# Kernel tuning notes

Measured on AMD Instinct MI355X. Metric: run time of the kernel, lower is better.

Reference implementation:

```python
import jax, jax.numpy as jnp
import numpy as np

T, V, D, L, H, F, R = 1024, 17, 1024, 2, 16, 4096, 32
DH = D // H
LORA_SCALE = 2.0  # lora_alpha / r = 64 / 32
MASK_ID = 16
NEG = jnp.float32(-1e9)


def setup_inputs() -> dict:
    key = jax.random.key(0)
    ks = iter(jax.random.split(key, 64))
    def p(shape, std):
        return jax.random.normal(next(ks), shape, jnp.float32) * std
    inp = {
        "packed_context": jax.random.randint(next(ks), (T,), 0, V),
        "cu_seq_lens": jnp.sort(jax.random.randint(next(ks), (5,), 0, T)),
        "max_seq_len": T,
        "row_coords": jax.random.randint(next(ks), (T,), 0, 64),
        "col_coords": jax.random.randint(next(ks), (T,), 0, 64),
        "num_diffusion_steps": 2,
        "E": p((V, D), 0.02),  # embed rows actually used: weight[:vocab_size]
    }
    shapes = {"q": (D, D), "k": (D, D), "v": (D, D), "o": (D, D),
              "g": (D, F), "u": (D, F), "d": (F, D)}
    for nm, (di, do) in shapes.items():
        inp["W" + nm] = p((L, di, do), di ** -0.5)  # frozen NF4 base weight (dequantized)
        inp["A" + nm] = p((L, di, R), di ** -0.5)   # LoRA A
        inp["B" + nm] = p((L, R, do), 0.01)          # LoRA B (nonzero for grad testing)
    inp["ln1"] = jnp.ones((L, D), jnp.float32)
    inp["ln2"] = jnp.ones((L, D), jnp.float32)
    inp["lnf"] = jnp.ones((D,), jnp.float32)
    return inp


def _rms(x, w):
    return x * jax.lax.rsqrt(jnp.mean(x * x, axis=-1, keepdims=True) + 1e-6) * w


def _lora(x, W, A, B):
    # fused base matmul + low-rank LoRA delta
    return x @ W + LORA_SCALE * ((x @ A) @ B)


def _denoise_step(soft, E, Wq, Aq, Bq, Wk, Ak, Bk, Wv, Av, Bv, Wo, Ao, Bo,
                  Wg, Ag, Bg, Wu, Au, Bu, Wd, Ad, Bd, ln1, ln2, lnf, causal_bias):
    # soft-token embedding: [T,V] @ [V,D]
    x = soft @ E
    inv_sqrt_dh = jnp.float32(1.0 / np.sqrt(DH))
    for l in range(L):
        h = _rms(x, ln1[l])
        q = _lora(h, Wq[l], Aq[l], Bq[l]).reshape(T, H, DH)
        k = _lora(h, Wk[l], Ak[l], Bk[l]).reshape(T, H, DH)
        v = _lora(h, Wv[l], Av[l], Bv[l]).reshape(T, H, DH)
        scores = jnp.einsum('qhd,khd->hqk', q, k) * inv_sqrt_dh + causal_bias
        att = jax.nn.softmax(scores, axis=-1)
        ctx = jnp.einsum('hqk,khd->qhd', att, v).reshape(T, D)
        x = x + _lora(ctx, Wo[l], Ao[l], Bo[l])
        h2 = _rms(x, ln2[l])
        ff = jax.nn.silu(_lora(h2, Wg[l], Ag[l], Bg[l])) * _lora(h2, Wu[l], Au[l], Bu[l])
        x = x + _lora(ff, Wd[l], Ad[l], Bd[l])
    logits = _rms(x, lnf) @ E.T  # tied head over the 17-token task vocab
    return jax.nn.softmax(logits, axis=-1)


def reference(packed_context, cu_seq_lens, max_seq_len, row_coords, col_coords,
              num_diffusion_steps, E, Wq, Aq, Bq, Wk, Ak, Bk, Wv, Av, Bv,
              Wo, Ao, Bo, Wg, Ag, Bg, Wu, Au, Bu, Wd, Ad, Bd, ln1, ln2, lnf):
    causal_bias = jnp.where(jnp.tril(jnp.ones((T, T), bool)), jnp.float32(0.0), NEG)
    is_prompt = (packed_context != MASK_ID)[:, None]  # [T,1]
    ctx_onehot = jax.nn.one_hot(packed_context, V, dtype=jnp.float32)
    soft = jnp.zeros((T, V), jnp.float32).at[:, MASK_ID].set(1.0)
    for _ in range(int(num_diffusion_steps)):
        refined = _denoise_step(soft, E, Wq, Aq, Bq, Wk, Ak, Bk, Wv, Av, Bv,
                                Wo, Ao, Bo, Wg, Ag, Bg, Wu, Au, Bu, Wd, Ad, Bd,
                                ln1, ln2, lnf, causal_bias)
        soft = jnp.where(is_prompt, ctx_onehot, refined)
    return jnp.argmax(soft, axis=-1)
```

## Files before the change

kernel.cpp:

```cpp
#include <hip/hip_runtime.h>
#include <hip/hip_bf16.h>

#define T_LEN 1024
#define D_DIM 1024
#define V_DIM 17
#define H_NUM 16
#define DH_DIM 64
#define F_DIM 4096
#define R_LORA 32
#define N_LAYERS 2
#define N_STEPS 2
#define MASK_ID 16
#define LORA_SCALE 2.0f

typedef __attribute__((ext_vector_type(8))) short bfx8;
typedef __attribute__((ext_vector_type(4))) float f32x4;

typedef unsigned short ushort_t;
typedef unsigned int uint_t;

#define AS1 __attribute__((address_space(1)))
#define AS3 __attribute__((address_space(3)))

__device__ __forceinline__ void gload16(const ushort_t* g, ushort_t* l) {
    __builtin_amdgcn_global_load_lds((const AS1 void*)(const void*)g,
                                     (AS3 void*)(void*)l, 16, 0, 0);
}

__device__ __forceinline__ ushort_t f2bf(float v) {
    __hip_bfloat16 h = __float2bfloat16(v);
    return __builtin_bit_cast(unsigned short, h);
}
__device__ __forceinline__ float bf2f(ushort_t u) {
    return __uint_as_float(((uint_t)u) << 16);
}
__device__ __forceinline__ void split4_store(float y0, float y1, float y2, float y3,
                                             ushort_t* __restrict__ hi, ushort_t* __restrict__ lo,
                                             size_t idx) {
    ushort_t h0 = f2bf(y0), h1 = f2bf(y1), h2 = f2bf(y2), h3 = f2bf(y3);
    ushort_t l0 = f2bf(y0 - bf2f(h0));
    ushort_t l1 = f2bf(y1 - bf2f(h1));
    ushort_t l2 = f2bf(y2 - bf2f(h2));
    ushort_t l3 = f2bf(y3 - bf2f(h3));
    uint2 hv, lv;
    hv.x = (uint_t)h0 | ((uint_t)h1 << 16);
    hv.y = (uint_t)h2 | ((uint_t)h3 << 16);
    lv.x = (uint_t)l0 | ((uint_t)l1 << 16);
    lv.y = (uint_t)l2 | ((uint_t)l3 << 16);
    *(uint2*)(hi + idx) = hv;
    *(uint2*)(lo + idx) = lv;
}

__global__ void init_soft_kernel(float* __restrict__ soft) {
    int idx = blockIdx.x * blockDim.x + threadIdx.x;
    if (idx < T_LEN * V_DIM) {
        soft[idx] = ((idx % V_DIM) == MASK_ID) ? 1.0f : 0.0f;
    }
}

__global__ __launch_bounds__(256) void embed_kernel(const float* __restrict__ soft,
                                                    const float* __restrict__ E,
                                                    float* __restrict__ x) {
    int t = blockIdx.x;
    __shared__ float srow[V_DIM];
    if (threadIdx.x < V_DIM) srow[threadIdx.x] = soft[t * V_DIM + threadIdx.x];
    __syncthreads();
    for (int d = threadIdx.x; d < D_DIM; d += 256) {
        float acc = 0.f;
        #pragma unroll
        for (int v = 0; v < V_DIM; v++) acc += srow[v] * E[v * D_DIM + d];
        x[(size_t)t * D_DIM + d] = acc;
    }
}

__global__ __launch_bounds__(256) void fold_kernel(
    const float* __restrict__ W,
    const float* __restrict__ A,
    const float* __restrict__ Bm,
    ushort_t* __restrict__ oHi,
    ushort_t* __restrict__ oLo,
    int K, int N)
{
    const int l = blockIdx.z;
    W   += (size_t)l * K * N;
    A   += (size_t)l * K * R_LORA;
    Bm  += (size_t)l * R_LORA * N;
    oHi += (size_t)l * K * N;
    oLo += (size_t)l * K * N;
    __shared__ uint_t tile[64][65];
    const int tid = threadIdx.x;
    const int n0 = blockIdx.x * 64, k0 = blockIdx.y * 64;
    {
        const int nl = tid & 63, kq = tid >> 6;
        float breg[R_LORA];
        #pragma unroll
        for (int r = 0; r < R_LORA; r++) breg[r] = Bm[(size_t)r * N + n0 + nl];
        for (int i = 0; i < 16; i++) {
            const int kl = kq * 16 + i;
            const size_t kgl = (size_t)(k0 + kl);
            const float* arow = A + kgl * R_LORA;
            float acc = 0.f;
            #pragma unroll
            for (int r = 0; r < R_LORA; r++) acc = fmaf(arow[r], breg[r], acc);
            float val = W[kgl * N + n0 + nl] + LORA_SCALE * acc;
            ushort_t h = f2bf(val);
            ushort_t l2 = f2bf(val - bf2f(h));
            tile[kl][nl] = ((uint_t)h << 16) | (uint_t)l2;
        }
    }
    __syncthreads();
    {
        const int kl = tid & 63, nb = tid >> 6;
        for (int i = 0; i < 16; i++) {
            const int nl = nb * 16 + i;
            uint_t pk = tile[kl][nl];
            size_t idx = (size_t)(n0 + nl) * K + k0 + kl;
            oHi[idx] = (ushort_t)(pk >> 16);
            oLo[idx] = (ushort_t)(pk & 0xffffu);
        }
    }
}

__global__ __launch_bounds__(256) void rms_split_kernel(
    const float* __restrict__ x, const float* __restrict__ w,
    ushort_t* __restrict__ hi, ushort_t* __restrict__ lo)
{
    const int t = blockIdx.x, tid = threadIdx.x;
    const float* xr = x + (size_t)t * D_DIM;
    float4 xv = *(const float4*)(xr + tid * 4);
    float ss = xv.x * xv.x + xv.y * xv.y + xv.z * xv.z + xv.w * xv.w;
    __shared__ float red[4];
    const int lane = tid & 63, wv = tid >> 6;
    #pragma unroll
    for (int off = 32; off > 0; off >>= 1) ss += __shfl_xor(ss, off);
    if (lane == 0) red[wv] = ss;
    __syncthreads();
    ss = red[0] + red[1] + red[2] + red[3];
    const float r = 1.0f / sqrtf(ss * (1.0f / D_DIM) + 1e-6f);
    const float4 wv4 = *(const float4*)(w + tid * 4);
    size_t base = (size_t)t * D_DIM + tid * 4;
    split4_store(xv.x * r * wv4.x, xv.y * r * wv4.y, xv.z * r * wv4.z, xv.w * r * wv4.w,
                 hi, lo, base);
}

struct GemmJob {
    const ushort_t* Bh;
    const ushort_t* Bl;
    float* Cf;
    ushort_t* Ch;
    ushort_t* Cl;
    int k0, k1;
};

__global__ __launch_bounds__(256) void gemm128_kernel(
    const ushort_t* __restrict__ Ahi, const ushort_t* __restrict__ Alo,
    int K, int N, GemmJob j0, GemmJob j1, GemmJob j2, GemmJob j3)
{
    GemmJob jb = (blockIdx.z == 0) ? j0 : (blockIdx.z == 1) ? j1 : (blockIdx.z == 2) ? j2 : j3;
    __shared__ ushort_t Ash[128][32];
    __shared__ ushort_t Asl[128][32];
    __shared__ ushort_t Bsh[128][32];
    __shared__ ushort_t Bsl[128][32];

    const int tid = threadIdx.x, lane = tid & 63, w = tid >> 6;
    const int l15 = lane & 15, lg = lane >> 4;
    const int m0 = blockIdx.y * 128, n0 = blockIdx.x * 128;
    const int wm = (w >> 1) * 64, wn = (w & 1) * 64;

    const int r0 = w * 32;
    const int rsub = lane >> 2;
    const int cs = lane & 3;
    const int csl = (cs ^ (rsub & 3)) * 8;
    const int rsl = (lg ^ (l15 & 3)) * 8;

    f32x4 acc[4][4];
    #pragma unroll
    for (int i = 0; i < 4; i++)
        #pragma unroll
        for (int j = 0; j < 4; j++) acc[i][j] = f32x4{0.f, 0.f, 0.f, 0.f};

    const size_t rowA = (size_t)(m0 + r0 + rsub) * K;
    const size_t rowB = (size_t)(n0 + r0 + rsub) * K;
    const size_t rstep = (size_t)16 * K;

    for (int kk = jb.k0; kk < jb.k1; kk += 32) {
        {
            const ushort_t* a0 = Ahi + rowA + kk + csl;
            const ushort_t* a1 = Alo + rowA + kk + csl;
            const ushort_t* b0 = jb.Bh + rowB + kk + csl;
            const ushort_t* b1 = jb.Bl + rowB + kk + csl;
            gload16(a0,         &Ash[r0][0]);
            gload16(a0 + rstep, &Ash[r0 + 16][0]);
            gload16(a1,         &Asl[r0][0]);
            gload16(a1 + rstep, &Asl[r0 + 16][0]);
            gload16(b0,         &Bsh[r0][0]);
            gload16(b0 + rstep, &Bsh[r0 + 16][0]);
            gload16(b1,         &Bsl[r0][0]);
            gload16(b1 + rstep, &Bsl[r0 + 16][0]);
        }
        __syncthreads();
        bfx8 bh[4], bl[4];
        #pragma unroll
        for (int ni = 0; ni < 4; ni++) {
            bh[ni] = *(const bfx8*)&Bsh[wn + ni * 16 + l15][rsl];
            bl[ni] = *(const bfx8*)&Bsl[wn + ni * 16 + l15][rsl];
        }
        #pragma unroll
        for (int mi = 0; mi < 4; mi++) {
            bfx8 ah = *(const bfx8*)&Ash[wm + mi * 16 + l15][rsl];
            bfx8 al = *(const bfx8*)&Asl[wm + mi * 16 + l15][rsl];
            #pragma unroll
            for (int ni = 0; ni < 4; ni++) {
                acc[mi][ni] = __builtin_amdgcn_mfma_f32_16x16x32_bf16(ah, bh[ni], acc[mi][ni], 0, 0, 0);
                acc[mi][ni] = __builtin_amdgcn_mfma_f32_16x16x32_bf16(ah, bl[ni], acc[mi][ni], 0, 0, 0);
                acc[mi][ni] = __builtin_amdgcn_mfma_f32_16x16x32_bf16(al, bh[ni], acc[mi][ni], 0, 0, 0);
            }
        }
        __syncthreads();
    }

    if (jb.Cf) {
        #pragma unroll
        for (int mi = 0; mi < 4; mi++)
            #pragma unroll
            for (int ni = 0; ni < 4; ni++) {
                int col = n0 + wn + ni * 16 + l15;
                #pragma unroll
                for (int i = 0; i < 4; i++) {
                    int row = m0 + wm + mi * 16 + lg * 4 + i;
                    jb.Cf[(size_t)row * N + col] = acc[mi][ni][i];
                }
            }
    } else {
        #pragma unroll
        for (int mi = 0; mi < 4; mi++)
            #pragma unroll
            for (int ni = 0; ni < 4; ni++) {
                int col = n0 + wn + ni * 16 + l15;
                #pragma unroll
                for (int i = 0; i < 4; i++) {
                    int row = m0 + wm + mi * 16 + lg * 4 + i;
                    size_t idx = (size_t)row * N + col;
                    float v = acc[mi][ni][i];
                    ushort_t h = f2bf(v);
                    jb.Ch[idx] = h;
                    jb.Cl[idx] = f2bf(v - bf2f(h));
                }
            }
    }
}

__global__ void add2_kernel(float* __restrict__ x, const float* __restrict__ p0,
                            const float* __restrict__ p1, int n4) {
    int i = blockIdx.x * blockDim.x + threadIdx.x;
    if (i < n4) {
        float4 xv = *(const float4*)(x + (size_t)i * 4);
        float4 a = *(const float4*)(p0 + (size_t)i * 4);
        float4 b = *(const float4*)(p1 + (size_t)i * 4);
        xv.x += a.x + b.x; xv.y += a.y + b.y; xv.z += a.z + b.z; xv.w += a.w + b.w;
        *(float4*)(x + (size_t)i * 4) = xv;
    }
}
__global__ void add4_kernel(float* __restrict__ x, const float* __restrict__ p0,
                            const float* __restrict__ p1, const float* __restrict__ p2,
                            const float* __restrict__ p3, int n4) {
    int i = blockIdx.x * blockDim.x + threadIdx.x;
    if (i < n4) {
        float4 xv = *(const float4*)(x + (size_t)i * 4);
        float4 a = *(const float4*)(p0 + (size_t)i * 4);
        float4 b = *(const float4*)(p1 + (size_t)i * 4);
        float4 c = *(const float4*)(p2 + (size_t)i * 4);
        float4 d = *(const float4*)(p3 + (size_t)i * 4);
        xv.x += a.x + b.x + c.x + d.x;
        xv.y += a.y + b.y + c.y + d.y;
        xv.z += a.z + b.z + c.z + d.z;
        xv.w += a.w + b.w + c.w + d.w;
        *(float4*)(x + (size_t)i * 4) = xv;
    }
}

#define KS_PAD 72
#define P_PAD 72
__global__ __launch_bounds__(256, 1) void attn_mfma_kernel(
    const ushort_t* __restrict__ qh, const ushort_t* __restrict__ ql,
    const ushort_t* __restrict__ kh, const ushort_t* __restrict__ kl,
    const ushort_t* __restrict__ vh, const ushort_t* __restrict__ vl,
    ushort_t* __restrict__ chi, ushort_t* __restrict__ clo)
{
    __shared__ ushort_t Ksh[64][KS_PAD];
    __shared__ ushort_t Ksl[64][KS_PAD];
    __shared__ ushort_t VTh[64][KS_PAD];
    __shared__ ushort_t VTl[64][KS_PAD];
    __shared__ ushort_t Ph[4][16][P_PAD];
    __shared__ ushort_t Pl[4][16][P_PAD];

    const int qt = blockIdx.x, hh = blockIdx.y;
    const int tid = threadIdx.x, w = tid >> 6, lane = tid & 63;
    const int l15 = lane & 15, lg = lane >> 4;
    const int q0 = qt * 64;
    const int hcol = hh * DH_DIM;

    bfx8 qa_h[2], qa_l[2];
    {
        size_t qrow = (size_t)(q0 + w * 16 + l15) * D_DIM + hcol;
        #pragma unroll
        for (int ks = 0; ks < 2; ks++) {
            qa_h[ks] = *(const bfx8*)(qh + qrow + ks * 32 + lg * 8);
            qa_l[ks] = *(const bfx8*)(ql + qrow + ks * 32 + lg * 8);
        }
    }

    f32x4 o[4];
    #pragma unroll
    for (int ni = 0; ni < 4; ni++) o[ni] = f32x4{0.f, 0.f, 0.f, 0.f};
    float mrun[4], lrun[4];
    #pragma unroll
    for (int i = 0; i < 4; i++) { mrun[i] = -3.0e38f; lrun[i] = 0.f; }

    const int srow = tid >> 2;
    const int sseg = (tid & 3) * 16;
    const int vp = tid & 31;
    const int vd0 = (tid >> 5) * 8;

    for (int kt = 0; kt <= qt; kt++) {
        __syncthreads();
        {
            size_t src = (size_t)(kt * 64 + srow) * D_DIM + hcol + sseg;
            *(uint4*)&Ksh[srow][sseg]     = *(const uint4*)(kh + src);
            *(uint4*)&Ksh[srow][sseg + 8] = *(const uint4*)(kh + src + 8);
            *(uint4*)&Ksl[srow][sseg]     = *(const uint4*)(kl + src);
            *(uint4*)&Ksl[srow][sseg + 8] = *(const uint4*)(kl + src + 8);
        }
        {
            size_t s0 = (size_t)(kt * 64 + 2 * vp) * D_DIM + hcol + vd0;
            uint4 h0 = *(const uint4*)(vh + s0);
            uint4 h1 = *(const uint4*)(vh + s0 + D_DIM);
            uint4 l0 = *(const uint4*)(vl + s0);
            uint4 l1 = *(const uint4*)(vl + s0 + D_DIM);
            const ushort_t* a = (const ushort_t*)&h0;
            const ushort_t* b = (const ushort_t*)&h1;
            const ushort_t* c = (const ushort_t*)&l0;
            const ushort_t* d = (const ushort_t*)&l1;
            #pragma unroll
            for (int j = 0; j < 8; j++) {
                *(uint_t*)&VTh[vd0 + j][2 * vp] = (uint_t)a[j] | ((uint_t)b[j] << 16);
                *(uint_t*)&VTl[vd0 + j][2 * vp] = (uint_t)c[j] | ((uint_t)d[j] << 16);
            }
        }
        __syncthreads();

        f32x4 s[4];
        #pragma unroll
        for (int ni = 0; ni < 4; ni++) s[ni] = f32x4{0.f, 0.f, 0.f, 0.f};
        #pragma unroll
        for (int ks = 0; ks < 2; ks++) {
            #pragma unroll
            for (int ni = 0; ni < 4; ni++) {
                bfx8 bh = *(const bfx8*)&Ksh[ni * 16 + l15][ks * 32 + lg * 8];
                bfx8 bl = *(const bfx8*)&Ksl[ni * 16 + l15][ks * 32 + lg * 8];
                s[ni] = __builtin_amdgcn_mfma_f32_16x16x32_bf16(qa_h[ks], bh, s[ni], 0, 0, 0);
                s[ni] = __builtin_amdgcn_mfma_f32_16x16x32_bf16(qa_h[ks], bl, s[ni], 0, 0, 0);
                s[ni] = __builtin_amdgcn_mfma_f32_16x16x32_bf16(qa_l[ks], bh, s[ni], 0, 0, 0);
            }
        }

        const int kbase = kt * 64;
        float rmax[4];
        #pragma unroll
        for (int i = 0; i < 4; i++) rmax[i] = -3.0e38f;
        #pragma unroll
        for (int ni = 0; ni < 4; ni++) {
            int kc = kbase + ni * 16 + l15;
            #pragma unroll
            for (int i = 0; i < 4; i++) {
                int qrow = q0 + w * 16 + lg * 4 + i;
                float v = s[ni][i] * 0.125f;
                v = (kc <= qrow) ? v : -3.0e38f;
                s[ni][i] = v;
                rmax[i] = fmaxf(rmax[i], v);
            }
        }
        #pragma unroll
        for (int off = 1; off < 16; off <<= 1) {
            #pragma unroll
            for (int i = 0; i < 4; i++) rmax[i] = fmaxf(rmax[i], __shfl_xor(rmax[i], off));
        }
        float psum[4];
        #pragma unroll
        for (int i = 0; i < 4; i++) {
            float nm = fmaxf(mrun[i], rmax[i]);
            float sc = __expf(mrun[i] - nm);
            lrun[i] *= sc;
            #pragma unroll
            for (int ni = 0; ni < 4; ni++) o[ni][i] *= sc;
            mrun[i] = nm;
            psum[i] = 0.f;
        }
        #pragma unroll
        for (int ni = 0; ni < 4; ni++) {
            #pragma unroll
            for (int i = 0; i < 4; i++) {
                float e = __expf(s[ni][i] - mrun[i]);
                s[ni][i] = e;
                psum[i] += e;
            }
        }
        #pragma unroll
        for (int off = 1; off < 16; off <<= 1) {
            #pragma unroll
            for (int i = 0; i < 4; i++) psum[i] += __shfl_xor(psum[i], off);
        }
        #pragma unroll
        for (int i = 0; i < 4; i++) lrun[i] += psum[i];

        #pragma unroll
        for (int ni = 0; ni < 4; ni++) {
            #pragma unroll
            for (int i = 0; i < 4; i++) {
                float e = s[ni][i];
                ushort_t hp = f2bf(e);
                Ph[w][lg * 4 + i][ni * 16 + l15] = hp;
                Pl[w][lg * 4 + i][ni * 16 + l15] = f2bf(e - bf2f(hp));
            }
        }
        #pragma unroll
        for (int ks = 0; ks < 2; ks++) {
            bfx8 ah = *(const bfx8*)&Ph[w][l15][ks * 32 + lg * 8];
            bfx8 al = *(const bfx8*)&Pl[w][l15][ks * 32 + lg * 8];
            #pragma unroll
            for (int ni = 0; ni < 4; ni++) {
                bfx8 bh = *(const bfx8*)&VTh[ni * 16 + l15][ks * 32 + lg * 8];
                bfx8 bl = *(const bfx8*)&VTl[ni * 16 + l15][ks * 32 + lg * 8];
                o[ni] = __builtin_amdgcn_mfma_f32_16x16x32_bf16(ah, bh, o[ni], 0, 0, 0);
                o[ni] = __builtin_amdgcn_mfma_f32_16x16x32_bf16(ah, bl, o[ni], 0, 0, 0);
                o[ni] = __builtin_amdgcn_mfma_f32_16x16x32_bf16(al, bh, o[ni], 0, 0, 0);
            }
        }
    }

    #pragma unroll
    for (int i = 0; i < 4; i++) {
        float inv = 1.0f / lrun[i];
        #pragma unroll
        for (int ni = 0; ni < 4; ni++) o[ni][i] *= inv;
    }
    #pragma unroll
    for (int ni = 0; ni < 4; ni++) {
        int col = hcol + ni * 16 + l15;
        #pragma unroll
        for (int i = 0; i < 4; i++) {
            int row = q0 + w * 16 + lg * 4 + i;
            size_t idx = (size_t)row * D_DIM + col;
            float v = o[ni][i];
            ushort_t hp = f2bf(v);
            chi[idx] = hp;
            clo[idx] = f2bf(v - bf2f(hp));
        }
    }
}

__global__ void silu_split_kernel(const float* __restrict__ g, const float* __restrict__ u,
                                  ushort_t* __restrict__ hi, ushort_t* __restrict__ lo, int n4) {
    int i = blockIdx.x * blockDim.x + threadIdx.x;
    if (i < n4) {
        float4 gv = *(const float4*)(g + (size_t)i * 4);
        float4 uv = *(const float4*)(u + (size_t)i * 4);
        float y0 = gv.x / (1.f + expf(-gv.x)) * uv.x;
        float y1 = gv.y / (1.f + expf(-gv.y)) * uv.y;
        float y2 = gv.z / (1.f + expf(-gv.z)) * uv.z;
        float y3 = gv.w / (1.f + expf(-gv.w)) * uv.w;
        split4_store(y0, y1, y2, y3, hi, lo, (size_t)i * 4);
    }
}

__global__ __launch_bounds__(256) void head_kernel(const float* __restrict__ x,
                                                   const float* __restrict__ lnf,
                                                   const float* __restrict__ E,
                                                   const int* __restrict__ tok,
                                                   float* __restrict__ soft) {
    int t = blockIdx.x;
    int tid = threadIdx.x;
    __shared__ float y[D_DIM];
    __shared__ float red[4];
    __shared__ float logits[V_DIM];
    const float* xr = x + (size_t)t * D_DIM;
    float ss = 0.f;
    for (int d = tid; d < D_DIM; d += 256) { float v = xr[d]; ss += v * v; }
    int lane = tid & 63, wave = tid >> 6;
    for (int off = 32; off > 0; off >>= 1) ss += __shfl_xor(ss, off);
    if (lane == 0) red[wave] = ss;
    __syncthreads();
    ss = red[0] + red[1] + red[2] + red[3];
    float r = 1.0f / sqrtf(ss * (1.0f / D_DIM) + 1e-6f);
    for (int d = tid; d < D_DIM; d += 256) y[d] = xr[d] * r * lnf[d];
    __syncthreads();
    for (int vv = wave; vv < V_DIM; vv += 4) {
        float p = 0.f;
        for (int d = lane; d < D_DIM; d += 64) p += y[d] * E[vv * D_DIM + d];
        for (int off = 32; off > 0; off >>= 1) p += __shfl_xor(p, off);
        if (lane == 0) logits[vv] = p;
    }
    __syncthreads();
    if (tid == 0) {
        int tk = tok[t];
        if (tk != MASK_ID) {
            for (int vv = 0; vv < V_DIM; vv++) soft[t * V_DIM + vv] = (vv == tk) ? 1.f : 0.f;
        } else {
            float mx = -1e30f;
            for (int vv = 0; vv < V_DIM; vv++) mx = fmaxf(mx, logits[vv]);
            float sm = 0.f;
            float e[V_DIM];
            for (int vv = 0; vv < V_DIM; vv++) { e[vv] = expf(logits[vv] - mx); sm += e[vv]; }
            float invs = 1.0f / sm;
            for (int vv = 0; vv < V_DIM; vv++) soft[t * V_DIM + vv] = e[vv] * invs;
        }
    }
}

__global__ void argmax_kernel(const float* __restrict__ soft, int* __restrict__ out) {
    int t = blockIdx.x * blockDim.x + threadIdx.x;
    if (t < T_LEN) {
        const float* s = soft + t * V_DIM;
        int best = 0;
        float bv = s[0];
        #pragma unroll
        for (int vv = 1; vv < V_DIM; vv++) {
            float v = s[vv];
            if (v > bv) { bv = v; best = vv; }
        }
        out[t] = best;
    }
}

__global__ __launch_bounds__(256) void rms_kernel(const float* __restrict__ x,
                                                  const float* __restrict__ w,
                                                  float* __restrict__ out) {
    int t = blockIdx.x;
    const float* xr = x + (size_t)t * D_DIM;
    float ss = 0.f;
    for (int d = threadIdx.x; d < D_DIM; d += 256) { float v = xr[d]; ss += v * v; }
    __shared__ float red[4];
    int lane = threadIdx.x & 63, wave = threadIdx.x >> 6;
    for (int off = 32; off > 0; off >>= 1) ss += __shfl_xor(ss, off);
    if (lane == 0) red[wave] = ss;
    __syncthreads();
    ss = red[0] + red[1] + red[2] + red[3];
    float r = 1.0f / sqrtf(ss * (1.0f / D_DIM) + 1e-6f);
    for (int d = threadIdx.x; d < D_DIM; d += 256) out[(size_t)t * D_DIM + d] = xr[d] * r * w[d];
}

__global__ __launch_bounds__(256) void gemm_kernel(const float* __restrict__ A,
                                                   const float* __restrict__ B,
                                                   float* __restrict__ C,
                                                   int M, int N, int K,
                                                   float alpha, int accumulate) {
    const int BM = 64, BN = 64, BK = 16;
    __shared__ float As[BK][BM];
    __shared__ float Bsh[BK][BN];
    int tid = threadIdx.x;
    int tx = tid % 16, ty = tid / 16;
    int row0 = blockIdx.y * BM, col0 = blockIdx.x * BN;
    float acc[4][4] = {};
    for (int k0 = 0; k0 < K; k0 += BK) {
        #pragma unroll
        for (int i = 0; i < 4; i++) {
            int e = tid * 4 + i;
            int m = e / BK, kk = e % BK;
            int gr = row0 + m, gk = k0 + kk;
            As[kk][m] = (gr < M && gk < K) ? A[(size_t)gr * K + gk] : 0.f;
        }
        #pragma unroll
        for (int i = 0; i < 4; i++) {
            int e = tid * 4 + i;
            int kk = e / BN, n = e % BN;
            int gk = k0 + kk, gc = col0 + n;
            Bsh[kk][n] = (gk < K && gc < N) ? B[(size_t)gk * N + gc] : 0.f;
        }
        __syncthreads();
        #pragma unroll
        for (int kk = 0; kk < BK; kk++) {
            float a[4], b[4];
            #pragma unroll
            for (int i = 0; i < 4; i++) a[i] = As[kk][ty * 4 + i];
            #pragma unroll
            for (int j = 0; j < 4; j++) b[j] = Bsh[kk][tx * 4 + j];
            #pragma unroll
            for (int i = 0; i < 4; i++)
                #pragma unroll
                for (int j = 0; j < 4; j++)
                    acc[i][j] += a[i] * b[j];
        }
        __syncthreads();
    }
    #pragma unroll
    for (int i = 0; i < 4; i++) {
        int r = row0 + ty * 4 + i;
        if (r >= M) continue;
        #pragma unroll
        for (int j = 0; j < 4; j++) {
            int c = col0 + tx * 4 + j;
            if (c >= N) continue;
            size_t idx = (size_t)r * N + c;
            float val = alpha * acc[i][j];
            if (accumulate) val += C[idx];
            C[idx] = val;
        }
    }
}

__global__ __launch_bounds__(256) void attn_kernel(const float* __restrict__ q,
                                                   const float* __restrict__ k,
                                                   const float* __restrict__ v,
                                                   float* __restrict__ ctx) {
    int qi = blockIdx.x;
    int hh = blockIdx.y;
    __shared__ float sc[T_LEN];
    __shared__ float qrow[DH_DIM];
    __shared__ float red[8];
    __shared__ float part[4][DH_DIM];
    int tid = threadIdx.x;
    int lane = tid & 63, wave = tid >> 6;
    const float* qp = q + (size_t)qi * D_DIM + hh * DH_DIM;
    if (tid < DH_DIM) qrow[tid] = qp[tid];
    __syncthreads();
    const float scale = 0.125f;
    for (int j = wave; j <= qi; j += 4) {
        const float* kp = k + (size_t)j * D_DIM + hh * DH_DIM;
        float p = qrow[lane] * kp[lane];
        for (int off = 32; off > 0; off >>= 1) p += __shfl_xor(p, off);
        if (lane == 0) sc[j] = p * scale;
    }
    __syncthreads();
    int n = qi + 1;
    float m = -1e30f;
    for (int j = tid; j < n; j += 256) m = fmaxf(m, sc[j]);
    for (int off = 32; off > 0; off >>= 1) m = fmaxf(m, __shfl_xor(m, off));
    if (lane == 0) red[wave] = m;
    __syncthreads();
    m = fmaxf(fmaxf(red[0], red[1]), fmaxf(red[2], red[3]));
    float s = 0.f;
    for (int j = tid; j < n; j += 256) { float e = expf(sc[j] - m); sc[j] = e; s += e; }
    for (int off = 32; off > 0; off >>= 1) s += __shfl_xor(s, off);
    if (lane == 0) red[4 + wave] = s;
    __syncthreads();
    s = red[4] + red[5] + red[6] + red[7];
    float inv = 1.0f / s;
    float acc = 0.f;
    for (int j = wave; j < n; j += 4) {
        acc += sc[j] * v[(size_t)j * D_DIM + hh * DH_DIM + lane];
    }
    part[wave][lane] = acc;
    __syncthreads();
    if (tid < DH_DIM) {
        float r = (part[0][tid] + part[1][tid] + part[2][tid] + part[3][tid]) * inv;
        ctx[(size_t)qi * D_DIM + hh * DH_DIM + tid] = r;
    }
}

__global__ void silu_mul_kernel(const float* __restrict__ g, const float* __restrict__ u,
                                float* __restrict__ out, int nelem) {
    int i = blockIdx.x * blockDim.x + threadIdx.x;
    if (i < nelem) {
        float gv = g[i];
        float sg = 1.0f / (1.0f + expf(-gv));
        out[i] = gv * sg * u[i];
    }
}

static inline void launch_gemm(const float* A, const float* B, float* C,
                               int M, int N, int K, float alpha, int accumulate,
                               hipStream_t stream) {
    dim3 grid((N + 63) / 64, (M + 63) / 64);
    gemm_kernel<<<grid, 256, 0, stream>>>(A, B, C, M, N, K, alpha, accumulate);
}

extern "C" void kernel_launch(void* const* d_in, const int* in_sizes, int n_in,
                              void* d_out, int out_size, void* d_ws, size_t ws_size,
                              hipStream_t stream) {
    const int* packed = (const int*)d_in[0];
    const float* E  = (const float*)d_in[6];
    const float* Wsrc[7] = {(const float*)d_in[7],  (const float*)d_in[10], (const float*)d_in[13],
                            (const float*)d_in[16], (const float*)d_in[19], (const float*)d_in[22],
                            (const float*)d_in[25]};
    const float* Asrc[7] = {(const float*)d_in[8],  (const float*)d_in[11], (const float*)d_in[14],
                            (const float*)d_in[17], (const float*)d_in[20], (const float*)d_in[23],
                            (const float*)d_in[26]};
    const float* Bsrc[7] = {(const float*)d_in[9],  (const float*)d_in[12], (const float*)d_in[15],
                            (const float*)d_in[18], (const float*)d_in[21], (const float*)d_in[24],
                            (const float*)d_in[27]};
    const float* ln1 = (const float*)d_in[28];
    const float* ln2 = (const float*)d_in[29];
    const float* lnf = (const float*)d_in[30];

    const size_t DD = (size_t)D_DIM * D_DIM;
    const size_t DF = (size_t)D_DIM * F_DIM;
    const size_t wsizes[7] = {DD, DD, DD, DD, DF, DF, DF};
    const int Kdim[7] = {D_DIM, D_DIM, D_DIM, D_DIM, D_DIM, D_DIM, F_DIM};
    const int Ndim[7] = {D_DIM, D_DIM, D_DIM, D_DIM, F_DIM, F_DIM, D_DIM};

    size_t u16_elems = 0;
    for (int p = 0; p < 7; p++) u16_elems += 2ull * N_LAYERS * wsizes[p];
    u16_elems += 2ull * DD;
    u16_elems += 2ull * DD;
    u16_elems += 2ull * DF;
    u16_elems += 6ull * DD;
    size_t f32_elems = (size_t)T_LEN * V_DIM + DD  + 2 * DF ;
    size_t need = u16_elems * 2 + f32_elems * 4 + 256;

    if (ws_size >= need) {
        ushort_t* ub = (ushort_t*)d_ws;
        size_t uo = 0;
        ushort_t *Whi[7], *Wlo[7];
        for (int p = 0; p < 7; p++) {
            Whi[p] = ub + uo; uo += (size_t)N_LAYERS * wsizes[p];
            Wlo[p] = ub + uo; uo += (size_t)N_LAYERS * wsizes[p];
        }
        ushort_t* h_hi = ub + uo; uo += DD;
        ushort_t* h_lo = ub + uo; uo += DD;
        ushort_t* c_hi = ub + uo; uo += DD;
        ushort_t* c_lo = ub + uo; uo += DD;
        ushort_t* f_hi = ub + uo; uo += DF;
        ushort_t* f_lo = ub + uo; uo += DF;
        ushort_t* qbh = ub + uo; uo += DD;
        ushort_t* qbl = ub + uo; uo += DD;
        ushort_t* kbh = ub + uo; uo += DD;
        ushort_t* kbl = ub + uo; uo += DD;
        ushort_t* vbh = ub + uo; uo += DD;
        ushort_t* vbl = ub + uo; uo += DD;
        float* fb = (float*)(ub + uo);
        size_t fo = 0;
        float* soft = fb + fo; fo += (size_t)T_LEN * V_DIM;
        float* x    = fb + fo; fo += DD;
        float* gbuf = fb + fo; fo += DF;
        float* ubuf = fb + fo; fo += DF;
        float* p0 = gbuf;
        float* p1 = gbuf + DD;
        float* p2 = gbuf + 2 * DD;
        float* p3 = gbuf + 3 * DD;

        for (int p = 0; p < 7; p++) {
            dim3 grid(Ndim[p] / 64, Kdim[p] / 64, N_LAYERS);
            fold_kernel<<<grid, 256, 0, stream>>>(Wsrc[p], Asrc[p], Bsrc[p],
                                                  Whi[p], Wlo[p], Kdim[p], Ndim[p]);
        }

        init_soft_kernel<<<(T_LEN * V_DIM + 255) / 256, 256, 0, stream>>>(soft);

        const int n4 = (int)(DD / 4);
        for (int step = 0; step < N_STEPS; step++) {
            embed_kernel<<<T_LEN, 256, 0, stream>>>(soft, E, x);
            for (int l = 0; l < N_LAYERS; l++) {
                rms_split_kernel<<<T_LEN, 256, 0, stream>>>(x, ln1 + (size_t)l * D_DIM, h_hi, h_lo);
                {
                    GemmJob jq = {Whi[0] + l * DD, Wlo[0] + l * DD, nullptr, qbh, qbl, 0, D_DIM};
                    GemmJob jk = {Whi[1] + l * DD, Wlo[1] + l * DD, nullptr, kbh, kbl, 0, D_DIM};
                    GemmJob jv = {Whi[2] + l * DD, Wlo[2] + l * DD, nullptr, vbh, vbl, 0, D_DIM};
                    gemm128_kernel<<<dim3(8, 8, 3), 256, 0, stream>>>(
                        h_hi, h_lo, D_DIM, D_DIM, jq, jk, jv, jq);
                }
                attn_mfma_kernel<<<dim3(T_LEN / 64, H_NUM), 256, 0, stream>>>(
                    qbh, qbl, kbh, kbl, vbh, vbl, c_hi, c_lo);
                {
                    const ushort_t* bh = Whi[3] + l * DD;
                    const ushort_t* bl = Wlo[3] + l * DD;
                    GemmJob ja = {bh, bl, p0, nullptr, nullptr, 0, 256};
                    GemmJob jb = {bh, bl, p1, nullptr, nullptr, 256, 512};
                    GemmJob jc = {bh, bl, p2, nullptr, nullptr, 512, 768};
                    GemmJob jd = {bh, bl, p3, nullptr, nullptr, 768, 1024};
                    gemm128_kernel<<<dim3(8, 8, 4), 256, 0, stream>>>(
                        c_hi, c_lo, D_DIM, D_DIM, ja, jb, jc, jd);
                    add4_kernel<<<(n4 + 255) / 256, 256, 0, stream>>>(x, p0, p1, p2, p3, n4);
                }
                rms_split_kernel<<<T_LEN, 256, 0, stream>>>(x, ln2 + (size_t)l * D_DIM, h_hi, h_lo);
                {
                    GemmJob jg = {Whi[4] + l * DF, Wlo[4] + l * DF, gbuf, nullptr, nullptr, 0, D_DIM};
                    GemmJob ju = {Whi[5] + l * DF, Wlo[5] + l * DF, ubuf, nullptr, nullptr, 0, D_DIM};
                    gemm128_kernel<<<dim3(32, 8, 2), 256, 0, stream>>>(
                        h_hi, h_lo, D_DIM, F_DIM, jg, ju, jg, jg);
                }
                silu_split_kernel<<<(T_LEN * F_DIM / 4 + 255) / 256, 256, 0, stream>>>(
                    gbuf, ubuf, f_hi, f_lo, T_LEN * F_DIM / 4);
                {
                    const ushort_t* bh = Whi[6] + l * DF;
                    const ushort_t* bl = Wlo[6] + l * DF;
                    GemmJob ja = {bh, bl, p0, nullptr, nullptr, 0, 1024};
                    GemmJob jb = {bh, bl, p1, nullptr, nullptr, 1024, 2048};
                    GemmJob jc = {bh, bl, p2, nullptr, nullptr, 2048, 3072};
                    GemmJob jd = {bh, bl, p3, nullptr, nullptr, 3072, 4096};
                    gemm128_kernel<<<dim3(8, 8, 4), 256, 0, stream>>>(
                        f_hi, f_lo, F_DIM, D_DIM, ja, jb, jc, jd);
                    add4_kernel<<<(n4 + 255) / 256, 256, 0, stream>>>(x, p0, p1, p2, p3, n4);
                }
            }
            head_kernel<<<T_LEN, 256, 0, stream>>>(x, lnf, E, packed, soft);
        }
        argmax_kernel<<<(T_LEN + 255) / 256, 256, 0, stream>>>(soft, (int*)d_out);
        return;
    }

    float* ws = (float*)d_ws;
    size_t off = 0;
    float* soft = ws + off; off += (size_t)T_LEN * V_DIM;
    float* x    = ws + off; off += (size_t)T_LEN * D_DIM;
    float* h    = ws + off; off += (size_t)T_LEN * D_DIM;
    float* qb   = ws + off; off += (size_t)T_LEN * D_DIM;
    float* kb   = ws + off; off += (size_t)T_LEN * D_DIM;
    float* vb   = ws + off; off += (size_t)T_LEN * D_DIM;
    float* cb   = ws + off; off += (size_t)T_LEN * D_DIM;
    float* gb   = ws + off; off += (size_t)T_LEN * F_DIM;
    float* ubf  = ws + off; off += (size_t)T_LEN * F_DIM;
    float* tmp  = ws + off; off += (size_t)T_LEN * R_LORA;

    init_soft_kernel<<<(T_LEN * V_DIM + 255) / 256, 256, 0, stream>>>(soft);
    for (int step = 0; step < N_STEPS; step++) {
        embed_kernel<<<T_LEN, 256, 0, stream>>>(soft, E, x);
        for (int l = 0; l < N_LAYERS; l++) {
            const float* ln1_l = ln1 + (size_t)l * D_DIM;
            const float* ln2_l = ln2 + (size_t)l * D_DIM;
            rms_kernel<<<T_LEN, 256, 0, stream>>>(x, ln1_l, h);
            launch_gemm(h, Asrc[0] + (size_t)l * D_DIM * R_LORA, tmp, T_LEN, R_LORA, D_DIM, 1.0f, 0, stream);
            launch_gemm(h, Wsrc[0] + (size_t)l * DD, qb, T_LEN, D_DIM, D_DIM, 1.0f, 0, stream);
            launch_gemm(tmp, Bsrc[0] + (size_t)l * R_LORA * D_DIM, qb, T_LEN, D_DIM, R_LORA, LORA_SCALE, 1, stream);
            launch_gemm(h, Asrc[1] + (size_t)l * D_DIM * R_LORA, tmp, T_LEN, R_LORA, D_DIM, 1.0f, 0, stream);
            launch_gemm(h, Wsrc[1] + (size_t)l * DD, kb, T_LEN, D_DIM, D_DIM, 1.0f, 0, stream);
            launch_gemm(tmp, Bsrc[1] + (size_t)l * R_LORA * D_DIM, kb, T_LEN, D_DIM, R_LORA, LORA_SCALE, 1, stream);
            launch_gemm(h, Asrc[2] + (size_t)l * D_DIM * R_LORA, tmp, T_LEN, R_LORA, D_DIM, 1.0f, 0, stream);
            launch_gemm(h, Wsrc[2] + (size_t)l * DD, vb, T_LEN, D_DIM, D_DIM, 1.0f, 0, stream);
            launch_gemm(tmp, Bsrc[2] + (size_t)l * R_LORA * D_DIM, vb, T_LEN, D_DIM, R_LORA, LORA_SCALE, 1, stream);
            attn_kernel<<<dim3(T_LEN, H_NUM), 256, 0, stream>>>(qb, kb, vb, cb);
            launch_gemm(cb, Asrc[3] + (size_t)l * D_DIM * R_LORA, tmp, T_LEN, R_LORA, D_DIM, 1.0f, 0, stream);
            launch_gemm(cb, Wsrc[3] + (size_t)l * DD, x, T_LEN, D_DIM, D_DIM, 1.0f, 1, stream);
            launch_gemm(tmp, Bsrc[3] + (size_t)l * R_LORA * D_DIM, x, T_LEN, D_DIM, R_LORA, LORA_SCALE, 1, stream);
            rms_kernel<<<T_LEN, 256, 0, stream>>>(x, ln2_l, h);
            launch_gemm(h, Asrc[4] + (size_t)l * D_DIM * R_LORA, tmp, T_LEN, R_LORA, D_DIM, 1.0f, 0, stream);
            launch_gemm(h, Wsrc[4] + (size_t)l * DF, gb, T_LEN, F_DIM, D_DIM, 1.0f, 0, stream);
            launch_gemm(tmp, Bsrc[4] + (size_t)l * R_LORA * F_DIM, gb, T_LEN, F_DIM, R_LORA, LORA_SCALE, 1, stream);
            launch_gemm(h, Asrc[5] + (size_t)l * D_DIM * R_LORA, tmp, T_LEN, R_LORA, D_DIM, 1.0f, 0, stream);
            launch_gemm(h, Wsrc[5] + (size_t)l * DF, ubf, T_LEN, F_DIM, D_DIM, 1.0f, 0, stream);
            launch_gemm(tmp, Bsrc[5] + (size_t)l * R_LORA * F_DIM, ubf, T_LEN, F_DIM, R_LORA, LORA_SCALE, 1, stream);
            silu_mul_kernel<<<(T_LEN * F_DIM + 255) / 256, 256, 0, stream>>>(gb, ubf, gb, T_LEN * F_DIM);
            launch_gemm(gb, Asrc[6] + (size_t)l * F_DIM * R_LORA, tmp, T_LEN, R_LORA, F_DIM, 1.0f, 0, stream);
            launch_gemm(gb, Wsrc[6] + (size_t)l * DF, x, T_LEN, D_DIM, F_DIM, 1.0f, 1, stream);
            launch_gemm(tmp, Bsrc[6] + (size_t)l * R_LORA * D_DIM, x, T_LEN, D_DIM, R_LORA, LORA_SCALE, 1, stream);
        }
        head_kernel<<<T_LEN, 256, 0, stream>>>(x, lnf, E, packed, soft);
    }
    argmax_kernel<<<(T_LEN + 255) / 256, 256, 0, stream>>>(soft, (int*)d_out);
}
```

Before: 1.247 ms.

## Fuse residual add with RMSNorm, vectorize fold kernel, retune LDS swizzle

Merges the split-K partial-sum residual add with the following RMSNorm-and-split step into a single kernel, which saves one full read and write of the activation per fusion point. The weight-fold kernel now reads its LoRA A rows as float4 and writes the transposed output with 16-byte vector stores instead of scattered 2-byte stores. The GEMM's LDS XOR swizzle now keys on row pairs, aimed at reducing bank conflicts. The swizzle change alters the shared-memory addressing pattern and could add conflicts if it is mismatched with the read path.

Result: no change. 1.229 ms (-1.4%).

```diff
diff --git a/kernel.cpp b/kernel.cpp
--- a/kernel.cpp
+++ b/kernel.cpp
@@ -98,10 +98,16 @@
         for (int i = 0; i < 16; i++) {
             const int kl = kq * 16 + i;
             const size_t kgl = (size_t)(k0 + kl);
-            const float* arow = A + kgl * R_LORA;
+            const float4* arow4 = (const float4*)(A + kgl * R_LORA);
             float acc = 0.f;
             #pragma unroll
-            for (int r = 0; r < R_LORA; r++) acc = fmaf(arow[r], breg[r], acc);
+            for (int r4 = 0; r4 < 8; r4++) {
+                float4 a = arow4[r4];
+                acc = fmaf(a.x, breg[r4 * 4 + 0], acc);
+                acc = fmaf(a.y, breg[r4 * 4 + 1], acc);
+                acc = fmaf(a.z, breg[r4 * 4 + 2], acc);
+                acc = fmaf(a.w, breg[r4 * 4 + 3], acc);
+            }
             float val = W[kgl * N + n0 + nl] + LORA_SCALE * acc;
             ushort_t h = f2bf(val);
             ushort_t l2 = f2bf(val - bf2f(h));
@@ -110,14 +116,20 @@
     }
     __syncthreads();
     {
-        const int kl = tid & 63, nb = tid >> 6;
+        const int nl = tid >> 2;
+        const int kc0 = (tid & 3) * 16;
+        ushort_t hb[16], lb[16];
+        #pragma unroll
         for (int i = 0; i < 16; i++) {
-            const int nl = nb * 16 + i;
-            uint_t pk = tile[kl][nl];
-            size_t idx = (size_t)(n0 + nl) * K + k0 + kl;
-            oHi[idx] = (ushort_t)(pk >> 16);
-            oLo[idx] = (ushort_t)(pk & 0xffffu);
-        }
+            uint_t pk = tile[kc0 + i][nl];
+            hb[i] = (ushort_t)(pk >> 16);
+            lb[i] = (ushort_t)(pk & 0xffffu);
+        }
+        size_t idx = (size_t)(n0 + nl) * K + k0 + kc0;
+        *(uint4*)(oHi + idx)     = *(uint4*)&hb[0];
+        *(uint4*)(oHi + idx + 8) = *(uint4*)&hb[8];
+        *(uint4*)(oLo + idx)     = *(uint4*)&lb[0];
+        *(uint4*)(oLo + idx + 8) = *(uint4*)&lb[8];
     }
 }
 
@@ -143,6 +155,37 @@
                  hi, lo, base);
 }
 
+__global__ __launch_bounds__(256) void add4_rms_split_kernel(
+    float* __restrict__ x, const float* __restrict__ p0, const float* __restrict__ p1,
+    const float* __restrict__ p2, const float* __restrict__ p3,
+    const float* __restrict__ w, ushort_t* __restrict__ hi, ushort_t* __restrict__ lo)
+{
+    const int t = blockIdx.x, tid = threadIdx.x;
+    size_t base = (size_t)t * D_DIM + tid * 4;
+    float4 xv = *(const float4*)(x + base);
+    float4 a = *(const float4*)(p0 + base);
+    float4 b = *(const float4*)(p1 + base);
+    float4 c = *(const float4*)(p2 + base);
+    float4 d = *(const float4*)(p3 + base);
+    xv.x += a.x + b.x + c.x + d.x;
+    xv.y += a.y + b.y + c.y + d.y;
+    xv.z += a.z + b.z + c.z + d.z;
+    xv.w += a.w + b.w + c.w + d.w;
+    *(float4*)(x + base) = xv;
+    float ss = xv.x * xv.x + xv.y * xv.y + xv.z * xv.z + xv.w * xv.w;
+    __shared__ float red[4];
+    const int lane = tid & 63, wv = tid >> 6;
+    #pragma unroll
+    for (int off = 32; off > 0; off >>= 1) ss += __shfl_xor(ss, off);
+    if (lane == 0) red[wv] = ss;
+    __syncthreads();
+    ss = red[0] + red[1] + red[2] + red[3];
+    const float r = 1.0f / sqrtf(ss * (1.0f / D_DIM) + 1e-6f);
+    const float4 wv4 = *(const float4*)(w + tid * 4);
+    split4_store(xv.x * r * wv4.x, xv.y * r * wv4.y, xv.z * r * wv4.z, xv.w * r * wv4.w,
+                 hi, lo, base);
+}
+
 struct GemmJob {
     const ushort_t* Bh;
     const ushort_t* Bl;
@@ -170,8 +213,8 @@
     const int r0 = w * 32;
     const int rsub = lane >> 2;
     const int cs = lane & 3;
-    const int csl = (cs ^ (rsub & 3)) * 8;
-    const int rsl = (lg ^ (l15 & 3)) * 8;
+    const int csl = (cs ^ ((rsub >> 1) & 3)) * 8;
+    const int rsl = (lg ^ ((l15 >> 1) & 3)) * 8;
 
     f32x4 acc[4][4];
     #pragma unroll
@@ -250,17 +293,6 @@
     }
 }
 
-__global__ void add2_kernel(float* __restrict__ x, const float* __restrict__ p0,
-                            const float* __restrict__ p1, int n4) {
-    int i = blockIdx.x * blockDim.x + threadIdx.x;
-    if (i < n4) {
-        float4 xv = *(const float4*)(x + (size_t)i * 4);
-        float4 a = *(const float4*)(p0 + (size_t)i * 4);
-        float4 b = *(const float4*)(p1 + (size_t)i * 4);
-        xv.x += a.x + b.x; xv.y += a.y + b.y; xv.z += a.z + b.z; xv.w += a.w + b.w;
-        *(float4*)(x + (size_t)i * 4) = xv;
-    }
-}
 __global__ void add4_kernel(float* __restrict__ x, const float* __restrict__ p0,
                             const float* __restrict__ p1, const float* __restrict__ p2,
                             const float* __restrict__ p3, int n4) {
@@ -749,8 +781,8 @@
         const int n4 = (int)(DD / 4);
         for (int step = 0; step < N_STEPS; step++) {
             embed_kernel<<<T_LEN, 256, 0, stream>>>(soft, E, x);
+            rms_split_kernel<<<T_LEN, 256, 0, stream>>>(x, ln1, h_hi, h_lo);
             for (int l = 0; l < N_LAYERS; l++) {
-                rms_split_kernel<<<T_LEN, 256, 0, stream>>>(x, ln1 + (size_t)l * D_DIM, h_hi, h_lo);
                 {
                     GemmJob jq = {Whi[0] + l * DD, Wlo[0] + l * DD, nullptr, qbh, qbl, 0, D_DIM};
                     GemmJob jk = {Whi[1] + l * DD, Wlo[1] + l * DD, nullptr, kbh, kbl, 0, D_DIM};
@@ -769,9 +801,9 @@
                     GemmJob jd = {bh, bl, p3, nullptr, nullptr, 768, 1024};
                     gemm128_kernel<<<dim3(8, 8, 4), 256, 0, stream>>>(
                         c_hi, c_lo, D_DIM, D_DIM, ja, jb, jc, jd);
-                    add4_kernel<<<(n4 + 255) / 256, 256, 0, stream>>>(x, p0, p1, p2, p3, n4);
+                    add4_rms_split_kernel<<<T_LEN, 256, 0, stream>>>(
+                        x, p0, p1, p2, p3, ln2 + (size_t)l * D_DIM, h_hi, h_lo);
                 }
-                rms_split_kernel<<<T_LEN, 256, 0, stream>>>(x, ln2 + (size_t)l * D_DIM, h_hi, h_lo);
                 {
                     GemmJob jg = {Whi[4] + l * DF, Wlo[4] + l * DF, gbuf, nullptr, nullptr, 0, D_DIM};
                     GemmJob ju = {Whi[5] + l * DF, Wlo[5] + l * DF, ubuf, nullptr, nullptr, 0, D_DIM};
@@ -789,7 +821,12 @@
                     GemmJob jd = {bh, bl, p3, nullptr, nullptr, 3072, 4096};
                     gemm128_kernel<<<dim3(8, 8, 4), 256, 0, stream>>>(
                         f_hi, f_lo, F_DIM, D_DIM, ja, jb, jc, jd);
-                    add4_kernel<<<(n4 + 255) / 256, 256, 0, stream>>>(x, p0, p1, p2, p3, n4);
+                    if (l + 1 < N_LAYERS) {
+                        add4_rms_split_kernel<<<T_LEN, 256, 0, stream>>>(
+                            x, p0, p1, p2, p3, ln1 + (size_t)(l + 1) * D_DIM, h_hi, h_lo);
+                    } else {
+                        add4_kernel<<<(n4 + 255) / 256, 256, 0, stream>>>(x, p0, p1, p2, p3, n4);
+                    }
                 }
             }
             head_kernel<<<T_LEN, 256, 0, stream>>>(x, lnf, E, packed, soft);
```
